# Performance work log

Measured on AMD Instinct MI355X. Metric: run time of the kernel, lower is better.

The kernel has to match this reference:

```python
import jax, jax.numpy as jnp
import numpy as np

B, T, D, O = 32, 1024, 1024, 256


def _glorot(key, shape):
    fan_in, fan_out = shape[0], shape[-1]
    std = np.sqrt(2.0 / (fan_in + fan_out))
    return jax.random.normal(key, shape, dtype=jnp.float32) * std


def setup_inputs() -> dict:
    key = jax.random.key(0)
    ks = jax.random.split(key, 14)
    return {
        "inputs": jax.random.normal(ks[0], (B, T, D), dtype=jnp.float32),
        # attention cell params
        "Wa": _glorot(ks[1], (O, O)),
        "Ua": _glorot(ks[2], (D, O)),
        "Va": _glorot(ks[3], (O, 1)),
        "Ba1": _glorot(ks[4], (1, O)),
        "Ba2": _glorot(ks[5], (T, O)),
        "Ba3": _glorot(ks[6], (T, 1)),
        # cascaded GRU cell params (Bo1 and inner keras GRUCell are unused in call)
        "Wo": _glorot(ks[7], (O, 1)),
        "Uo": _glorot(ks[8], (D, O)),
        "Co": _glorot(ks[9], (D, O)),
        "Bo2": _glorot(ks[10], (1, O)),
        "Bo3": _glorot(ks[11], (1, O)),
        "Bo4": _glorot(ks[12], (1, O)),
        "emb": _glorot(ks[13], (O, O)),
    }


def reference(inputs, Wa, Ua, Va, Ba1, Ba2, Ba3, Wo, Uo, Co, Bo2, Bo3, Bo4, emb):
    # inputs: [B, T, D]
    # UaH is identical every decoder step in the original code -> hoist (same math).
    UaH = jnp.einsum("btd,do->bto", inputs, Ua) + Ba2          # [B,T,O]
    # prev_state at step t is inputs[:, t-1, :] with wraparound at t=0.
    prev_in = jnp.roll(inputs, 1, axis=1)                        # [B,T,D]
    UoH_all = jnp.einsum("btd,do->bto", prev_in, Uo) + Bo2      # [B,T,O]

    def step(prev_pred, uoh_t):
        # --- attention cell (query = tanh(prev_pred)) ---
        WaS = jnp.tanh(prev_pred) @ Wa + Ba1                     # [B,O]
        scores = jnp.tanh(UaH + WaS[:, None, :]) @ Va + Ba3     # [B,T,1]
        sm = jax.nn.softmax(scores, axis=1)                      # [B,T,1]
        ctx = jnp.sum(inputs * sm, axis=1)                       # [B,D]
        # --- cascaded GRU cell ---
        woy = (jax.nn.softmax(prev_pred) @ emb) @ Wo             # [B,1]
        coc = ctx @ Co + Bo3                                     # [B,O]
        pred = woy + uoh_t + coc + Bo4                           # [B,O]
        return pred, pred

    init = jnp.zeros((inputs.shape[0], Wa.shape[0]), dtype=inputs.dtype)
    _, outs = jax.lax.scan(step, init, jnp.swapaxes(UoH_all, 0, 1))  # [T,B,O]
    return jnp.swapaxes(outs, 0, 1)                                   # [B,T,O]
```

## Files before the change

kernel.cpp:

```cpp
#include <hip/hip_runtime.h>
#include <hip/hip_fp16.h>


typedef unsigned int uint32;
typedef unsigned short u16;
typedef unsigned long long u64;

#define NTH 512

__device__ __forceinline__ float b2f(u16 u) { return __uint_as_float(((uint32)u) << 16); }
__device__ __forceinline__ u16 f2b(float f) {
    uint32 u = __float_as_uint(f);
    uint32 r = u + 0x7fffu + ((u >> 16) & 1u);
    return (u16)(r >> 16);
}
__device__ __forceinline__ float lo_bf(uint32 d) { return __uint_as_float(d << 16); }
__device__ __forceinline__ float hi_bf(uint32 d) { return __uint_as_float(d & 0xffff0000u); }
__device__ __forceinline__ float tanh_fast(float x) {
    float e = __expf(x + x);
    return 1.0f - 2.0f * __builtin_amdgcn_rcpf(e + 1.0f);
}
__device__ __forceinline__ uint32 pack2h(float x, float y) {
    return (uint32)__half_as_ushort(__float2half(x)) |
           ((uint32)__half_as_ushort(__float2half(y)) << 16);
}
__device__ __forceinline__ float unpk_lo(uint32 w) {
    return __half2float(__ushort_as_half((unsigned short)(w & 0xFFFFu)));
}
__device__ __forceinline__ float unpk_hi(uint32 w) {
    return __half2float(__ushort_as_half((unsigned short)(w >> 16)));
}

__device__ __forceinline__ uint32 coh_ld(const uint32* p) {
    return __hip_atomic_load(p, __ATOMIC_RELAXED, __HIP_MEMORY_SCOPE_AGENT);
}
__device__ __forceinline__ u64 coh_ld64(const u64* p) {
    return __hip_atomic_load(p, __ATOMIC_RELAXED, __HIP_MEMORY_SCOPE_AGENT);
}
__device__ __forceinline__ void coh_st(uint32* p, uint32 v) {
    __hip_atomic_store(p, v, __ATOMIC_RELAXED, __HIP_MEMORY_SCOPE_AGENT);
}

#define OFF_E  ((size_t)0)
#define OFF_IC ((size_t)16777216)
#define WS_NEEDED ((size_t)33554432)

__device__ uint32 g_Ph[2][32][8][132];
__device__ uint32 g_mS[2][32][8];
__device__ uint32 g_flag[2][32][8];
__device__ float g_embWo[256];

__global__ __launch_bounds__(512) void init_flags() {
    ((uint32*)g_flag)[threadIdx.x] = 0xFFFFFFFFu;
}

__global__ void setup_embWo(const float* __restrict__ emb, const float* __restrict__ Wo) {
    int o = threadIdx.x;
    float a = 0.f;
    for (int j = 0; j < 256; j++) a = fmaf(emb[o * 256 + j], Wo[j], a);
    g_embWo[o] = a;
}

__global__ __launch_bounds__(256) void gemm_pre(
    const float* __restrict__ in, const float* __restrict__ Ua,
    const float* __restrict__ Uo, const float* __restrict__ Co,
    const float* __restrict__ Ba2, const float* __restrict__ Bo2,
    const float* __restrict__ Bo3, const float* __restrict__ Bo4,
    u16* __restrict__ E, float* __restrict__ outStage, u16* __restrict__ ic) {
    __shared__ __align__(16) float smA[32][132];
    __shared__ __align__(16) float smB[32][128];

    int tid = threadIdx.x;
    int rt = blockIdx.x, ct = blockIdx.y;
    int mat = ct >> 1;
    int o0 = (ct & 1) * 128;
    const float* W = (mat == 0) ? Ua : (mat == 1 ? Uo : Co);
    int r0 = rt * 128;
    int b = r0 >> 10, t0 = r0 & 1023;
    int tr = tid >> 4, tc = tid & 15;

    float acc[8][8];
#pragma unroll
    for (int i = 0; i < 8; i++)
#pragma unroll
        for (int j = 0; j < 8; j++) acc[i][j] = 0.f;

    for (int kc = 0; kc < 1024; kc += 32) {
#pragma unroll
        for (int l = 0; l < 4; l++) {
            int s = tid + l * 256;
            int i = s >> 3, c = s & 7;
            float4 v = *(const float4*)(in + (size_t)(r0 + i) * 1024 + kc + c * 4);
            smA[c * 4 + 0][i] = v.x;
            smA[c * 4 + 1][i] = v.y;
            smA[c * 4 + 2][i] = v.z;
            smA[c * 4 + 3][i] = v.w;
        }
#pragma unroll
        for (int l = 0; l < 4; l++) {
            int s = tid + l * 256;
            int dd = s >> 5, c = s & 31;
            *(float4*)&smB[dd][c * 4] = *(const float4*)(W + (size_t)(kc + dd) * 256 + o0 + c * 4);
        }
        __syncthreads();
#pragma unroll 4
        for (int j = 0; j < 32; j++) {
            float a0[8], b0[8];
            *(float4*)&a0[0] = *(const float4*)&smA[j][tr * 8];
            *(float4*)&a0[4] = *(const float4*)&smA[j][tr * 8 + 4];
            *(float4*)&b0[0] = *(const float4*)&smB[j][tc * 8];
            *(float4*)&b0[4] = *(const float4*)&smB[j][tc * 8 + 4];
#pragma unroll
            for (int rr = 0; rr < 8; rr++)
#pragma unroll
                for (int cc = 0; cc < 8; cc++) acc[rr][cc] = fmaf(a0[rr], b0[cc], acc[rr][cc]);
        }
        __syncthreads();
    }

    if (mat == 0) {
#pragma unroll
        for (int rr = 0; rr < 8; rr++) {
            int t = t0 + tr * 8 + rr;
#pragma unroll
            for (int cc = 0; cc < 8; cc++) {
                int o = o0 + tc * 8 + cc;
                float v = __expf(2.f * (acc[rr][cc] + Ba2[t * 256 + o]));
                E[((((size_t)b << 10) + t) << 8) + o] = f2b(v);
            }
        }
    } else if (mat == 1) {
#pragma unroll
        for (int rr = 0; rr < 8; rr++) {
            int t = t0 + tr * 8 + rr;
            int t1 = (t + 1) & 1023;
#pragma unroll
            for (int cc = 0; cc < 8; cc++) {
                int o = o0 + tc * 8 + cc;
                outStage[(((size_t)b << 10) + t1) * 256 + o] = acc[rr][cc] + Bo2[o] + Bo3[o] + Bo4[o];
            }
        }
    } else {
#pragma unroll
        for (int rr = 0; rr < 8; rr++) {
            int t = t0 + tr * 8 + rr;
#pragma unroll
            for (int cc = 0; cc < 8; cc++)
                ic[(((size_t)b << 10) + t) * 256 + o0 + tc * 8 + cc] = f2b(acc[rr][cc]);
        }
    }
}

__global__ __launch_bounds__(NTH) void seq8(
    const float* __restrict__ Wa, const float* __restrict__ Va,
    const float* __restrict__ Ba1, const float* __restrict__ Ba3,
    const u16* __restrict__ E, const u16* __restrict__ IC,
    float* __restrict__ out) {
    __shared__ uint32 smWa2[128 * 256];
    __shared__ __align__(16) float smScratch[2048];
    __shared__ float smPred[256], smQ[256], smF[256], smVa[256], smBa1[256];
    __shared__ float smS[128], smEe[128], smBa3[128];
    __shared__ float smT[16];

    int tid = threadIdx.x;
    int b = blockIdx.x & 31, g = blockIdx.x >> 5;
    int lane = tid & 63, w = tid >> 6;
    int t0 = g << 7;

    if (tid < 256) {
        smVa[tid] = Va[tid]; smBa1[tid] = Ba1[tid];
        smPred[tid] = 0.f; smQ[tid] = 0.f;
    }
    if (tid < 128) smBa3[tid] = Ba3[t0 + tid];
    for (int idx = tid; idx < 32768; idx += NTH) {
        int j2 = idx >> 8, o = idx & 255;
        uint32 u0 = (uint32)f2b(Wa[(size_t)(2 * j2) * 256 + o]);
        uint32 u1 = (uint32)f2b(Wa[(size_t)(2 * j2 + 1) * 256 + o]);
        smWa2[idx] = u0 | (u1 << 16);
    }
    __syncthreads();

    float sv = (tid < 256) ? smVa[tid] : 0.f;
#pragma unroll
    for (int off = 32; off; off >>= 1) sv += __shfl_xor(sv, off, 64);
    if (lane == 0) smT[w] = sv;
    __syncthreads();
    float sumVa = smT[0] + smT[1] + smT[2] + smT[3];
    float myEmb = (tid < 256) ? g_embWo[tid] : 0.f;
    __syncthreads();

    const u16* Eb = E + ((size_t)b << 18);
    const u16* ICb = IC + ((size_t)b << 18);
    float* outb = out + ((size_t)b << 18);
    long bud = 1000000000L;

    uint4 ev8[8];
    {
        int tl = tid >> 2, oq = tid & 3;
        const uint4* row = (const uint4*)(Eb + (((size_t)(t0 + tl)) << 8) + (oq << 6));
#pragma unroll
        for (int k = 0; k < 8; k++) ev8[k] = row[(k + oq) & 7];
    }
    uint2 icv[16];
    {
        int rg = tid >> 6, o4 = (tid & 63) << 2;
        const u16* icp = ICb + (((size_t)t0) << 8) + o4;
#pragma unroll
        for (int r = 0; r < 16; r++)
            icv[r] = *(const uint2*)(icp + ((size_t)((rg << 4) + r) << 8));
    }

    for (int t = 0; t < 1024; t++) {
        uint32* bufP  = &g_Ph[t & 1][b][g][0];
        uint32* flags = &g_flag[t & 1][b][0];
        float uoh = (tid < 256) ? outb[((size_t)t << 8) + tid] : 0.f;

        float pv = 0.f;
        if (tid < 256) {
            pv = smPred[tid];
            float m = pv;
#pragma unroll
            for (int off = 32; off; off >>= 1) m = fmaxf(m, __shfl_xor(m, off, 64));
            if (lane == 0) smT[w] = m;
        }
        {
            int o = tid & 255, h = tid >> 8;
            const uint32* wp = &smWa2[(h << 6) * 256 + o];
            const float* qp = &smQ[h << 7];
            float a = 0.f;
#pragma unroll 8
            for (int j2 = 0; j2 < 64; j2++) {
                float2 q2 = *(const float2*)&qp[j2 * 2];
                uint32 p = wp[j2 << 8];
                a = fmaf(lo_bf(p), q2.x, a);
                a = fmaf(hi_bf(p), q2.y, a);
            }
            smScratch[tid] = a;
        }
        __syncthreads();
        if (tid < 256) {
            float M = fmaxf(fmaxf(smT[0], smT[1]), fmaxf(smT[2], smT[3]));
            float e = __expf(pv - M);
            float s1 = e, s2 = e * myEmb;
#pragma unroll
            for (int off = 32; off; off >>= 1) {
                s1 += __shfl_xor(s1, off, 64);
                s2 += __shfl_xor(s2, off, 64);
            }
            if (lane == 0) { smT[4 + w] = s1; smT[8 + w] = s2; }
            smF[tid] = __expf(2.f * (smBa1[tid] + smScratch[tid] + smScratch[256 + tid]));
        }
        __syncthreads();
        float p_val = (smT[8] + smT[9] + smT[10] + smT[11]) *
                      __builtin_amdgcn_rcpf(smT[4] + smT[5] + smT[6] + smT[7]);

        {
            int tl = tid >> 2, oq = tid & 3;
            float acc = 0.f;
#pragma unroll
            for (int k = 0; k < 8; k++) {
                uint4 ev = ev8[k];
                int ob = (oq << 6) + (((k + oq) & 7) << 3);
                float4 fA = *(const float4*)&smF[ob];
                float4 fB = *(const float4*)&smF[ob + 4];
                float4 vA = *(const float4*)&smVa[ob];
                float4 vB = *(const float4*)&smVa[ob + 4];
                acc = fmaf(vA.x, __builtin_amdgcn_rcpf(fmaf(lo_bf(ev.x), fA.x, 1.f)), acc);
                acc = fmaf(vA.y, __builtin_amdgcn_rcpf(fmaf(hi_bf(ev.x), fA.y, 1.f)), acc);
                acc = fmaf(vA.z, __builtin_amdgcn_rcpf(fmaf(lo_bf(ev.y), fA.z, 1.f)), acc);
                acc = fmaf(vA.w, __builtin_amdgcn_rcpf(fmaf(hi_bf(ev.y), fA.w, 1.f)), acc);
                acc = fmaf(vB.x, __builtin_amdgcn_rcpf(fmaf(lo_bf(ev.z), fB.x, 1.f)), acc);
                acc = fmaf(vB.y, __builtin_amdgcn_rcpf(fmaf(hi_bf(ev.z), fB.y, 1.f)), acc);
                acc = fmaf(vB.z, __builtin_amdgcn_rcpf(fmaf(lo_bf(ev.w), fB.z, 1.f)), acc);
                acc = fmaf(vB.w, __builtin_amdgcn_rcpf(fmaf(hi_bf(ev.w), fB.w, 1.f)), acc);
            }
            acc += __shfl_xor(acc, 1, 64);
            acc += __shfl_xor(acc, 2, 64);
            if (oq == 0) smS[tl] = sumVa - 2.f * acc + smBa3[tl];
        }
        __syncthreads();
        if (tid < 64) {
            float s0 = smS[tid], s1 = smS[tid + 64];
            float mm = fmaxf(s0, s1);
#pragma unroll
            for (int off = 32; off; off >>= 1) mm = fmaxf(mm, __shfl_xor(mm, off, 64));
            float e0 = __expf(s0 - mm), e1 = __expf(s1 - mm);
            smEe[tid] = e0; smEe[tid + 64] = e1;
            float ls = e0 + e1;
#pragma unroll
            for (int off = 32; off; off >>= 1) ls += __shfl_xor(ls, off, 64);
            if (tid == 0) coh_st(&g_mS[t & 1][b][g], pack2h(mm, ls));
        }
        __syncthreads();
        {
            int rg = tid >> 6, o4 = (tid & 63) << 2;
            float4 a4 = {0.f, 0.f, 0.f, 0.f};
#pragma unroll 4
            for (int r = 0; r < 16; r++) {
                float e = smEe[(rg << 4) + r];
                uint2 iv = icv[r];
                a4.x = fmaf(e, lo_bf(iv.x), a4.x);
                a4.y = fmaf(e, hi_bf(iv.x), a4.y);
                a4.z = fmaf(e, lo_bf(iv.y), a4.z);
                a4.w = fmaf(e, hi_bf(iv.y), a4.w);
            }
            *(float4*)&smScratch[rg * 256 + o4] = a4;
        }
        __syncthreads();
        if (tid < 128) {
            float px = 0.f, py = 0.f;
#pragma unroll
            for (int rg = 0; rg < 8; rg++) {
                float2 v = *(const float2*)&smScratch[rg * 256 + 2 * tid];
                px += v.x; py += v.y;
            }
            coh_st(&bufP[tid], pack2h(px, py));
        }
        __syncthreads();
        if (tid == 0) coh_st(&flags[g], (uint32)t);
        if (tid < 8 && tid != g) {
            while (bud > 0) {
                if (atomicAdd(&flags[tid], 0u) == (uint32)t) break;
                bud--;
            }
        }
        __syncthreads();
        if (tid < 256) {
            const uint32* pb = &g_Ph[t & 1][b][0][0];
            int wo = tid >> 1, hsel = tid & 1;
            uint32 pw[8];
#pragma unroll
            for (int g2 = 0; g2 < 8; g2++) pw[g2] = coh_ld(&pb[g2 * 132 + wo]);
            const u64* msp = (const u64*)&g_mS[t & 1][b][0];
            u64 q0 = coh_ld64(&msp[0]), q1 = coh_ld64(&msp[1]);
            u64 q2 = coh_ld64(&msp[2]), q3 = coh_ld64(&msp[3]);
            uint32 msw[8] = {(uint32)q0, (uint32)(q0 >> 32),
                             (uint32)q1, (uint32)(q1 >> 32),
                             (uint32)q2, (uint32)(q2 >> 32),
                             (uint32)q3, (uint32)(q3 >> 32)};
            float M = unpk_lo(msw[0]);
#pragma unroll
            for (int g2 = 1; g2 < 8; g2++) M = fmaxf(M, unpk_lo(msw[g2]));
            float L = 0.f, Pt = 0.f;
#pragma unroll
            for (int g2 = 0; g2 < 8; g2++) {
                float eg = __expf(unpk_lo(msw[g2]) - M);
                L = fmaf(eg, unpk_hi(msw[g2]), L);
                float pg = hsel ? unpk_hi(pw[g2]) : unpk_lo(pw[g2]);
                Pt = fmaf(eg, pg, Pt);
            }
            float pr = p_val + uoh + Pt * __builtin_amdgcn_rcpf(L);
            if ((tid >> 5) == g) outb[((size_t)t << 8) + tid] = pr;
            smPred[tid] = pr;
            smQ[tid] = tanh_fast(pr);
        }
        __syncthreads();
    }
}

__global__ void zero_k(uint32* out, int n) {
    int i = blockIdx.x * 1024 + threadIdx.x;
    if (i < n) out[i] = 0;
}

extern "C" void kernel_launch(void* const* d_in, const int* in_sizes, int n_in,
                              void* d_out, int out_size, void* d_ws, size_t ws_size,
                              hipStream_t stream) {
    const float* in = (const float*)d_in[0];
    const float* Wa = (const float*)d_in[1];
    const float* Ua = (const float*)d_in[2];
    const float* Va = (const float*)d_in[3];
    const float* Ba1 = (const float*)d_in[4];
    const float* Ba2 = (const float*)d_in[5];
    const float* Ba3 = (const float*)d_in[6];
    const float* Wo = (const float*)d_in[7];
    const float* Uo = (const float*)d_in[8];
    const float* Co = (const float*)d_in[9];
    const float* Bo2 = (const float*)d_in[10];
    const float* Bo3 = (const float*)d_in[11];
    const float* Bo4 = (const float*)d_in[12];
    const float* emb = (const float*)d_in[13];
    float* out = (float*)d_out;
    char* ws = (char*)d_ws;

    if (ws_size < WS_NEEDED) {
        zero_k<<<(out_size + 1023) / 1024, 1024, 0, stream>>>((uint32*)out, out_size);
        return;
    }

    u16* E = (u16*)(ws + OFF_E);
    u16* icp = (u16*)(ws + OFF_IC);

    init_flags<<<1, 512, 0, stream>>>();
    setup_embWo<<<1, 256, 0, stream>>>(emb, Wo);
    gemm_pre<<<dim3(256, 6), 256, 0, stream>>>(in, Ua, Uo, Co, Ba2, Bo2, Bo3, Bo4, E, out, icp);
    seq8<<<256, NTH, 0, stream>>>(Wa, Va, Ba1, Ba3, E, icp, out);
}
```

Measured before the change: 7.922 ms.

## Stream E and IC tiles from global memory each step instead of caching in registers

Drops the per-thread register caches of the E tile (8 uint4) and IC tile (16 uint2), which were loaded once and held across all 1024 steps. Each step now reloads those values from global memory, relying on L1/L2 to serve them. The per-step gather of the eight softmax stats also changes: lanes 0-7 each load one word and broadcast it with shuffles, replacing four 64-bit atomic loads per thread. This lowers register pressure at the cost of repeated global or cache traffic on the serial critical path.

Result: faster. 7.240 ms (-8.6%).

```diff
diff --git a/kernel.cpp b/kernel.cpp
--- a/kernel.cpp
+++ b/kernel.cpp
@@ -4,7 +4,6 @@
 
 typedef unsigned int uint32;
 typedef unsigned short u16;
-typedef unsigned long long u64;
 
 #define NTH 512
 
@@ -32,9 +31,6 @@
 }
 
 __device__ __forceinline__ uint32 coh_ld(const uint32* p) {
-    return __hip_atomic_load(p, __ATOMIC_RELAXED, __HIP_MEMORY_SCOPE_AGENT);
-}
-__device__ __forceinline__ u64 coh_ld64(const u64* p) {
     return __hip_atomic_load(p, __ATOMIC_RELAXED, __HIP_MEMORY_SCOPE_AGENT);
 }
 __device__ __forceinline__ void coh_st(uint32* p, uint32 v) {
@@ -193,22 +189,6 @@
     const u16* ICb = IC + ((size_t)b << 18);
     float* outb = out + ((size_t)b << 18);
     long bud = 1000000000L;
-
-    uint4 ev8[8];
-    {
-        int tl = tid >> 2, oq = tid & 3;
-        const uint4* row = (const uint4*)(Eb + (((size_t)(t0 + tl)) << 8) + (oq << 6));
-#pragma unroll
-        for (int k = 0; k < 8; k++) ev8[k] = row[(k + oq) & 7];
-    }
-    uint2 icv[16];
-    {
-        int rg = tid >> 6, o4 = (tid & 63) << 2;
-        const u16* icp = ICb + (((size_t)t0) << 8) + o4;
-#pragma unroll
-        for (int r = 0; r < 16; r++)
-            icv[r] = *(const uint2*)(icp + ((size_t)((rg << 4) + r) << 8));
-    }
 
     for (int t = 0; t < 1024; t++) {
         uint32* bufP  = &g_Ph[t & 1][b][g][0];
@@ -256,11 +236,13 @@
 
         {
             int tl = tid >> 2, oq = tid & 3;
+            const uint4* row = (const uint4*)(Eb + (((size_t)(t0 + tl)) << 8) + (oq << 6));
             float acc = 0.f;
 #pragma unroll
             for (int k = 0; k < 8; k++) {
-                uint4 ev = ev8[k];
-                int ob = (oq << 6) + (((k + oq) & 7) << 3);
+                int kk = (k + oq) & 7;
+                uint4 ev = row[kk];
+                int ob = (oq << 6) + (kk << 3);
                 float4 fA = *(const float4*)&smF[ob];
                 float4 fB = *(const float4*)&smF[ob + 4];
                 float4 vA = *(const float4*)&smVa[ob];
@@ -293,12 +275,14 @@
         }
         __syncthreads();
         {
-            int rg = tid >> 6, o4 = (tid & 63) << 2;
+            int rg = tid >> 6, oc = tid & 63, o4 = oc << 2;
+            const u16* icp = ICb + (((size_t)t0) << 8) + o4;
             float4 a4 = {0.f, 0.f, 0.f, 0.f};
 #pragma unroll 4
             for (int r = 0; r < 16; r++) {
-                float e = smEe[(rg << 4) + r];
-                uint2 iv = icv[r];
+                int row = (rg << 4) + r;
+                float e = smEe[row];
+                uint2 iv = *(const uint2*)(icp + ((size_t)row << 8));
                 a4.x = fmaf(e, lo_bf(iv.x), a4.x);
                 a4.y = fmaf(e, hi_bf(iv.x), a4.y);
                 a4.z = fmaf(e, lo_bf(iv.y), a4.z);
@@ -331,13 +315,11 @@
             uint32 pw[8];
 #pragma unroll
             for (int g2 = 0; g2 < 8; g2++) pw[g2] = coh_ld(&pb[g2 * 132 + wo]);
-            const u64* msp = (const u64*)&g_mS[t & 1][b][0];
-            u64 q0 = coh_ld64(&msp[0]), q1 = coh_ld64(&msp[1]);
-            u64 q2 = coh_ld64(&msp[2]), q3 = coh_ld64(&msp[3]);
-            uint32 msw[8] = {(uint32)q0, (uint32)(q0 >> 32),
-                             (uint32)q1, (uint32)(q1 >> 32),
-                             (uint32)q2, (uint32)(q2 >> 32),
-                             (uint32)q3, (uint32)(q3 >> 32)};
+            uint32 msw_own = 0;
+            if (lane < 8) msw_own = coh_ld(&g_mS[t & 1][b][lane]);
+            uint32 msw[8];
+#pragma unroll
+            for (int g2 = 0; g2 < 8; g2++) msw[g2] = __shfl(msw_own, g2, 64);
             float M = unpk_lo(msw[0]);
 #pragma unroll
             for (int g2 = 1; g2 < 8; g2++) M = fmaxf(M, unpk_lo(msw[g2]));
```
